# Performance work log

Hardware: AMD Instinct MI355X
Metric: run time of the kernel (lower is better)

The kernel has to match this reference:

```python
import jax, jax.numpy as jnp
import numpy as np

N_NODES = 20000
N_EDGES = 640000
IN_DIM = 128
HID = 128
OUT_DIM = 64
N_STEPS = 16   # N in the torch module
H = 0.1        # ODE step size


def setup_inputs() -> dict:
    key = jax.random.key(0)
    ks = jax.random.split(key, 20)
    s = 1.0 / np.sqrt(HID)

    def g(k, shape, scale=s):
        return (jax.random.normal(k, shape, dtype=jnp.float32) * scale)

    return {
        "x": jax.random.normal(ks[0], (N_NODES, IN_DIM), dtype=jnp.float32),
        "edge_index": jax.random.randint(ks[1], (2, N_EDGES), 0, N_NODES, dtype=jnp.int32),
        "W_enc1": g(ks[2], (HID, IN_DIM), 1.0 / np.sqrt(IN_DIM)),
        "b_enc1": g(ks[3], (HID,)),
        "W_enc2": g(ks[4], (HID, HID)),
        "b_enc2": g(ks[5], (HID,)),
        "W_ih_f": g(ks[6], (4 * HID, HID)),
        "W_hh_f": g(ks[7], (4 * HID, HID)),
        "b_ih_f": g(ks[8], (4 * HID,)),
        "b_hh_f": g(ks[9], (4 * HID,)),
        "W_ih_b": g(ks[10], (4 * HID, HID)),
        "W_hh_b": g(ks[11], (4 * HID, HID)),
        "b_ih_b": g(ks[12], (4 * HID,)),
        "b_hh_b": g(ks[13], (4 * HID,)),
        "W_f1": g(ks[14], (HID, 2 * HID), 1.0 / np.sqrt(2 * HID)),
        "b_f1": g(ks[15], (HID,)),
        "W_f2": g(ks[16], (OUT_DIM, HID)),
        "b_f2": g(ks[17], (OUT_DIM,)),
    }


def _lstm_scan(xs, W_ih, W_hh, b_ih, b_hh):
    """Unidirectional LSTM over xs [T, B, H] -> hidden states [T, B, H]."""
    B = xs.shape[1]
    Hd = W_hh.shape[1]
    h0 = jnp.zeros((B, Hd), xs.dtype)

    def cell(carry, x_t):
        h, c = carry
        gates = x_t @ W_ih.T + b_ih + h @ W_hh.T + b_hh
        i, f, g, o = jnp.split(gates, 4, axis=-1)  # torch gate order: i,f,g,o
        i = jax.nn.sigmoid(i)
        f = jax.nn.sigmoid(f)
        g = jnp.tanh(g)
        o = jax.nn.sigmoid(o)
        c_new = f * c + i * g
        h_new = o * jnp.tanh(c_new)
        return (h_new, c_new), h_new

    _, hs = jax.lax.scan(cell, (h0, h0), xs)
    return hs


def reference(x, edge_index, W_enc1, b_enc1, W_enc2, b_enc2,
              W_ih_f, W_hh_f, b_ih_f, b_hh_f,
              W_ih_b, W_hh_b, b_ih_b, b_hh_b,
              W_f1, b_f1, W_f2, b_f2):
    row, col = edge_index[0], edge_index[1]

    # initial encoders
    X = x @ W_enc1.T + b_enc1
    Y = jnp.zeros_like(X)
    X = jax.nn.relu(X)
    X = X @ W_enc2.T + b_enc2

    # node degree (count of col occurrences), inf-guard not needed (deg used directly)
    deg = jax.ops.segment_sum(jnp.ones((N_EDGES,), X.dtype), col, num_segments=N_NODES)

    def wave_step(carry, _):
        Xc, Yc = carry
        # L x = deg*x - sum_{j->i} x_j   (scatter-add of -x[row] at col)
        mes = -jax.ops.segment_sum(Xc[row], col, num_segments=N_NODES)
        vel_update = deg[:, None] * Xc + mes
        Yn = Yc - H * vel_update
        Xn = Xc + H * Yn
        return (Xn, Yn), Xn

    _, Xs = jax.lax.scan(wave_step, (X, Y), None, length=N_STEPS - 1)
    X_tilde = jnp.concatenate([X[None], Xs], axis=0)  # [N, n_nodes, HID]

    hs_f = _lstm_scan(X_tilde, W_ih_f, W_hh_f, b_ih_f, b_hh_f)
    hs_b = _lstm_scan(X_tilde[::-1], W_ih_b, W_hh_b, b_ih_b, b_hh_b)
    # out_vec[-1] = [fwd hidden at last step, bwd hidden at last position]
    out_last = jnp.concatenate([hs_f[-1], hs_b[0]], axis=-1)  # [n_nodes, 2*HID]

    out = jax.nn.relu(out_last @ W_f1.T + b_f1)
    out = out @ W_f2.T + b_f2
    return out
```

## Files before the change

kernel.cpp:

```cpp
#include <hip/hip_runtime.h>
#include <hip/hip_bf16.h>
#include <cstdint>
#include <cstddef>

#define N_NODES 20000
#define N_EDGES 640000
#define HID     128
#define OUT_DIM 64
#define NSTEPS  16
#define HSTEP   0.1f
#define H2      0.01f
#define NBLK    625

typedef unsigned short u16;
typedef __attribute__((ext_vector_type(8))) short short8;
typedef __attribute__((ext_vector_type(4))) float f32x4;

__device__ __forceinline__ float bf2f(u16 u) {
    union { unsigned int i; float f; } v; v.i = ((unsigned int)u) << 16; return v.f;
}
__device__ __forceinline__ u16 f2bf(float f) {
    union { float f; unsigned int i; } v; v.f = f;
    unsigned int x = v.i;
    unsigned int r = x + 0x7FFFu + ((x >> 16) & 1u);
    return (u16)(r >> 16);
}

__device__ __forceinline__ float sigm(float x) { return 1.f / (1.f + __expf(-x)); }
__device__ __forceinline__ float tanh_fast(float x) {
    float e2 = __expf(-2.f * fabsf(x));
    float t = (1.f - e2) / (1.f + e2);
    return copysignf(t, x);
}

__global__ void detect_kernel(const u16* __restrict__ xraw, int* __restrict__ flag) {
    __shared__ int cnt;
    if (threadIdx.x == 0) cnt = 0;
    __syncthreads();
    int c = 0;
    for (int i = threadIdx.x; i < 4096; i += 256) {
        int e = (xraw[i] >> 7) & 0xFF;
        if (e >= 0x90) c++;
    }
    atomicAdd(&cnt, c);
    __syncthreads();
    if (threadIdx.x == 0) *flag = (cnt > 100) ? 1 : 0;
}

#define N_CVT 15
struct CvtArgs { const void* s[N_CVT]; };
__constant__ const int cvt_off[N_CVT + 1] = {
    0, 16384, 16512, 32896, 33024, 98560, 164096, 164608, 165120,
    230656, 231168, 231680, 264448, 264576, 272768, 272832 };

__global__ void convert_kernel(CvtArgs a, float* __restrict__ dst,
                               const int* __restrict__ flag) {
    int i = blockIdx.x * blockDim.x + threadIdx.x;
    if (i >= 272832) return;
    int seg = 0;
    #pragma unroll
    for (int s = 1; s < N_CVT; ++s) if (i >= cvt_off[s]) seg = s;
    int j = i - cvt_off[seg];
    float v = (*flag) ? ((const float*)a.s[seg])[j]
                      : bf2f(((const u16*)a.s[seg])[j]);
    dst[i] = v;
}

__global__ void build_wswz_kernel(const float* __restrict__ wsf,
                                  u16* __restrict__ WswzF, u16* __restrict__ WswzB,
                                  u16* __restrict__ WswzH, u16* __restrict__ WswzO,
                                  u16* __restrict__ WswzE1, u16* __restrict__ WswzE2) {
    int o = blockIdx.x * blockDim.x + threadIdx.x;
    if (o < 131072) {
        int j = o & 7, l = (o >> 3) & 63, rest = o >> 9;
        int ck = rest & 7, nt = rest >> 3;
        int n = nt * 16 + (l & 15);
        int k = ck * 32 + (l >> 4) * 8 + j;
        const float* Wihf = wsf + 33024;
        const float* Whhf = wsf + 98560;
        float v = (k < 128) ? Wihf[n * 128 + k] : Whhf[n * 128 + (k - 128)];
        WswzF[o] = f2bf(v);
    }
    if (o < 65536) {
        int j = o & 7, l = (o >> 3) & 63, rest = o >> 9;
        int ck = rest & 3, nt = rest >> 2;
        int n = nt * 16 + (l & 15);
        int k = ck * 32 + (l >> 4) * 8 + j;
        const float* Wihb = wsf + 165120;
        WswzB[o] = f2bf(Wihb[n * 128 + k]);
    }
    if (o < 32768) {
        int j = o & 7, l = (o >> 3) & 63, rest = o >> 9;
        int ck = rest & 7, nt = rest >> 3;
        int n = nt * 16 + (l & 15);
        int k = ck * 32 + (l >> 4) * 8 + j;
        const float* Wf1 = wsf + 231680;
        WswzH[o] = f2bf(Wf1[n * 256 + k]);
    }
    if (o < 8192) {
        int j = o & 7, l = (o >> 3) & 63, rest = o >> 9;
        int ck = rest & 3, nt = rest >> 2;
        int n = nt * 16 + (l & 15);
        int k = ck * 32 + (l >> 4) * 8 + j;
        const float* Wf2 = wsf + 264576;
        WswzO[o] = f2bf(Wf2[n * 128 + k]);
    }
    if (o < 16384) {
        int j = o & 7, l = (o >> 3) & 63, rest = o >> 9;
        int ck = rest & 3, nt = rest >> 2;
        int n = nt * 16 + (l & 15);
        int k = ck * 32 + (l >> 4) * 8 + j;
        const float* We1 = wsf + 0;
        const float* We2 = wsf + 16512;
        WswzE1[o] = f2bf(We1[n * 128 + k]);
        WswzE2[o] = f2bf(We2[n * 128 + k]);
    }
}

__global__ void count_kernel(const int* __restrict__ ei, int* __restrict__ deg) {
    int e = blockIdx.x * blockDim.x + threadIdx.x;
    if (e < N_EDGES) atomicAdd(&deg[ei[N_EDGES + e]], 1);
}

__global__ __launch_bounds__(1024) void scan_kernel(const int* __restrict__ deg,
                                                    int* __restrict__ rowptr,
                                                    float* __restrict__ degf) {
    __shared__ int sd[1024];
    const int t = threadIdx.x;
    const int CH = (N_NODES + 1023) / 1024;
    int base = t * CH;
    int s = 0;
    for (int i = 0; i < CH; ++i) {
        int idx = base + i;
        if (idx < N_NODES) s += deg[idx];
    }
    sd[t] = s;
    __syncthreads();
    for (int off = 1; off < 1024; off <<= 1) {
        int v = (t >= off) ? sd[t - off] : 0;
        __syncthreads();
        sd[t] += v;
        __syncthreads();
    }
    int run = (t == 0) ? 0 : sd[t - 1];
    for (int i = 0; i < CH; ++i) {
        int idx = base + i;
        if (idx < N_NODES) {
            rowptr[idx] = run;
            degf[idx] = (float)deg[idx];
            run += deg[idx];
        }
    }
    if (t == 1023) rowptr[N_NODES] = sd[1023];
}

__global__ void fill_kernel(const int* __restrict__ ei, const int* __restrict__ rowptr,
                            int* __restrict__ fill, int* __restrict__ csr) {
    int e = blockIdx.x * blockDim.x + threadIdx.x;
    if (e < N_EDGES) {
        int d = ei[N_EDGES + e];
        int p = atomicAdd(&fill[d], 1);
        csr[rowptr[d] + p] = ei[e];
    }
}

__global__ __launch_bounds__(512) void encoder_kernel(
    const void* __restrict__ xv,
    const u16* __restrict__ WswzE1, const u16* __restrict__ WswzE2,
    const float* __restrict__ benc1, const float* __restrict__ benc2,
    float* __restrict__ Xa, u16* __restrict__ Xsnap0, const int* __restrict__ flag)
{
    __shared__ __align__(16) u16 H1[32][136];
    const int w = threadIdx.x >> 6;
    const int l = threadIdx.x & 63;
    const int l15 = l & 15, quad = l >> 4;
    const int m0 = blockIdx.x * 32;
    const int kof = quad * 8;
    const int j = w * 16 + l15;
    const bool xf32 = (*flag != 0);

    f32x4 acc[2] = {};
    #pragma unroll
    for (int ck = 0; ck < 4; ++ck) {
        const int kc = ck * 32;
        short8 a0, a1;
        if (xf32) {
            const float* r0 = (const float*)xv + (size_t)(m0 + l15) * HID + kc + kof;
            const float* r1 = (const float*)xv + (size_t)(m0 + 16 + l15) * HID + kc + kof;
            union { u16 u[8]; short8 v; } t0, t1;
            #pragma unroll
            for (int e = 0; e < 8; ++e) { t0.u[e] = f2bf(r0[e]); t1.u[e] = f2bf(r1[e]); }
            a0 = t0.v; a1 = t1.v;
        } else {
            a0 = *(const short8*)((const u16*)xv + (size_t)(m0 + l15) * HID + kc + kof);
            a1 = *(const short8*)((const u16*)xv + (size_t)(m0 + 16 + l15) * HID + kc + kof);
        }
        short8 b = *(const short8*)(WswzE1 + (((size_t)(w * 4 + ck)) << 9) + (l << 3));
        acc[0] = __builtin_amdgcn_mfma_f32_16x16x32_bf16(a0, b, acc[0], 0, 0, 0);
        acc[1] = __builtin_amdgcn_mfma_f32_16x16x32_bf16(a1, b, acc[1], 0, 0, 0);
    }
    {
        const float bj = benc1[j];
        #pragma unroll
        for (int mt = 0; mt < 2; ++mt)
            #pragma unroll
            for (int i = 0; i < 4; ++i)
                H1[mt * 16 + quad * 4 + i][j] = f2bf(fmaxf(acc[mt][i] + bj, 0.f));
    }
    __syncthreads();

    f32x4 acc2[2] = {};
    #pragma unroll
    for (int ck = 0; ck < 4; ++ck) {
        const int kc = ck * 32;
        short8 a0 = *(const short8*)(&H1[l15][kc + kof]);
        short8 a1 = *(const short8*)(&H1[16 + l15][kc + kof]);
        short8 b = *(const short8*)(WswzE2 + (((size_t)(w * 4 + ck)) << 9) + (l << 3));
        acc2[0] = __builtin_amdgcn_mfma_f32_16x16x32_bf16(a0, b, acc2[0], 0, 0, 0);
        acc2[1] = __builtin_amdgcn_mfma_f32_16x16x32_bf16(a1, b, acc2[1], 0, 0, 0);
    }
    {
        const float bj = benc2[j];
        #pragma unroll
        for (int mt = 0; mt < 2; ++mt)
            #pragma unroll
            for (int i = 0; i < 4; ++i) {
                int m = m0 + mt * 16 + quad * 4 + i;
                float o = acc2[mt][i] + bj;
                Xa[(size_t)m * HID + j] = o;
                Xsnap0[(size_t)m * HID + j] = f2bf(o);
            }
    }
}

template<bool FIRST>
__global__ __launch_bounds__(256) void wave_kernel(
    const float* __restrict__ Xcur, float* __restrict__ Xdst,
    const u16* __restrict__ XbfP, u16* __restrict__ XbfN,
    const float* __restrict__ degf,
    const int* __restrict__ rowptr, const int* __restrict__ csr)
{
    const int node = blockIdx.x * 4 + (threadIdx.x >> 6);
    const int lane = threadIdx.x & 63;
    const int q = lane >> 4;
    const int fl = (lane & 15) * 8;

    const int beg = rowptr[node], end = rowptr[node + 1];
    float s0[8] = {}, s1[8] = {}, s2[8] = {}, s3[8] = {};

    int i = beg;
    for (; i + 16 <= end; i += 16) {
        int v0 = csr[i + 0 + q];
        int v1 = csr[i + 4 + q];
        int v2 = csr[i + 8 + q];
        int v3 = csr[i + 12 + q];
        short8 g0 = *(const short8*)(XbfP + (size_t)v0 * HID + fl);
        short8 g1 = *(const short8*)(XbfP + (size_t)v1 * HID + fl);
        short8 g2 = *(const short8*)(XbfP + (size_t)v2 * HID + fl);
        short8 g3 = *(const short8*)(XbfP + (size_t)v3 * HID + fl);
        #pragma unroll
        for (int e = 0; e < 8; ++e) {
            s0[e] += bf2f((u16)g0[e]);
            s1[e] += bf2f((u16)g1[e]);
            s2[e] += bf2f((u16)g2[e]);
            s3[e] += bf2f((u16)g3[e]);
        }
    }
    for (; i + 4 <= end; i += 4) {
        int v = csr[i + q];
        short8 g = *(const short8*)(XbfP + (size_t)v * HID + fl);
        #pragma unroll
        for (int e = 0; e < 8; ++e) s0[e] += bf2f((u16)g[e]);
    }
    if (i + q < end) {
        int v = csr[i + q];
        short8 g = *(const short8*)(XbfP + (size_t)v * HID + fl);
        #pragma unroll
        for (int e = 0; e < 8; ++e) s1[e] += bf2f((u16)g[e]);
    }

    float t[8];
    #pragma unroll
    for (int e = 0; e < 8; ++e) {
        t[e] = (s0[e] + s1[e]) + (s2[e] + s3[e]);
        t[e] += __shfl_xor(t[e], 16, 64);
        t[e] += __shfl_xor(t[e], 32, 64);
    }

    if (q == 0) {
        const size_t off = (size_t)node * HID + fl;
        float xc[8], xp[8], xn[8];
        *(float4*)&xc[0] = *(const float4*)(Xcur + off);
        *(float4*)&xc[4] = *(const float4*)(Xcur + off + 4);
        if (!FIRST) {
            *(float4*)&xp[0] = *(const float4*)(Xdst + off);
            *(float4*)&xp[4] = *(const float4*)(Xdst + off + 4);
        }
        const float d = degf[node];
        const float c0 = 2.f - H2 * d;
        short8 sv;
        #pragma unroll
        for (int e = 0; e < 8; ++e) {
            float prev = FIRST ? xc[e] : xp[e];
            xn[e] = c0 * xc[e] - prev + H2 * t[e];
            sv[e] = (short)f2bf(xn[e]);
        }
        *(float4*)(Xdst + off)     = *(float4*)&xn[0];
        *(float4*)(Xdst + off + 4) = *(float4*)&xn[4];
        *(short8*)(XbfN + off)     = sv;
    }
}

__global__ __launch_bounds__(512) void lstm16w_kernel(
    const u16* __restrict__ Xsnap,
    u16* __restrict__ hOut,
    const u16* __restrict__ WswzF,
    const float* __restrict__ bih, const float* __restrict__ bhh)
{
    __shared__ __align__(16) u16 hL[32][136];
    const int w = threadIdx.x >> 6;
    const int l = threadIdx.x & 63;
    const int l15 = l & 15, quad = l >> 4;
    const int m0 = blockIdx.x * 32;
    const int kof = quad * 8;
    const int j = w * 16 + l15;

    {
        const int r  = threadIdx.x >> 4;
        const int cc = (threadIdx.x & 15) * 8;
        short8 z = {};
        *(short8*)&hL[r][cc] = z;
    }

    short8 wf[4][8];
    #pragma unroll
    for (int q = 0; q < 4; ++q)
        #pragma unroll
        for (int ck = 0; ck < 8; ++ck)
            wf[q][ck] = *(const short8*)(WswzF +
                (((size_t)((q * 8 + w) * 8 + ck)) << 9) + (l << 3));

    const float bI = bih[j]       + bhh[j];
    const float bF = bih[128 + j] + bhh[128 + j];
    const float bG = bih[256 + j] + bhh[256 + j];
    const float bO = bih[384 + j] + bhh[384 + j];
    float cst[2][4] = {};

    const size_t rowA0 = (size_t)(m0 + l15) * HID + kof;
    const size_t rowA1 = (size_t)(m0 + 16 + l15) * HID + kof;
    __syncthreads();

    #pragma unroll 1
    for (int t = 0; t < NSTEPS; ++t) {
        const u16* Xbf = Xsnap + (size_t)t * N_NODES * HID;
        f32x4 acc[2][4] = {};
        #pragma unroll
        for (int ck = 0; ck < 8; ++ck) {
            const int kc = ck * 32;
            short8 a0, a1;
            if (kc < 128) {
                a0 = *(const short8*)(Xbf + rowA0 + kc);
                a1 = *(const short8*)(Xbf + rowA1 + kc);
            } else {
                a0 = *(const short8*)(&hL[l15][kc - 128 + kof]);
                a1 = *(const short8*)(&hL[16 + l15][kc - 128 + kof]);
            }
            #pragma unroll
            for (int q = 0; q < 4; ++q) {
                acc[0][q] = __builtin_amdgcn_mfma_f32_16x16x32_bf16(a0, wf[q][ck], acc[0][q], 0, 0, 0);
                acc[1][q] = __builtin_amdgcn_mfma_f32_16x16x32_bf16(a1, wf[q][ck], acc[1][q], 0, 0, 0);
            }
        }
        __syncthreads();
        #pragma unroll
        for (int mt = 0; mt < 2; ++mt) {
            #pragma unroll
            for (int i = 0; i < 4; ++i) {
                float gi = sigm(acc[mt][0][i] + bI);
                float gf = sigm(acc[mt][1][i] + bF);
                float gg = tanh_fast(acc[mt][2][i] + bG);
                float go = sigm(acc[mt][3][i] + bO);
                float cn = gf * cst[mt][i] + gi * gg;
                cst[mt][i] = cn;
                hL[mt * 16 + quad * 4 + i][j] = f2bf(go * tanh_fast(cn));
            }
        }
        __syncthreads();
    }

    {
        const int r  = threadIdx.x >> 4;
        const int cc = (threadIdx.x & 15) * 8;
        *(short8*)(hOut + (size_t)(m0 + r) * HID + cc) = *(const short8*)&hL[r][cc];
    }
}

__global__ __launch_bounds__(512) void tail2_kernel(
    const u16* __restrict__ Xbf15, const u16* __restrict__ h15,
    const u16* __restrict__ WswzB, const u16* __restrict__ WswzH,
    const u16* __restrict__ WswzO,
    const float* __restrict__ bihb, const float* __restrict__ bhhb,
    const float* __restrict__ bf1, const float* __restrict__ bf2_,
    void* __restrict__ out, const int* __restrict__ oflag)
{
    __shared__ __align__(16) u16 hL[32][136];
    __shared__ __align__(16) u16 Hb[32][136];
    __shared__ __align__(16) u16 F1[32][136];
    const int w = threadIdx.x >> 6;
    const int l = threadIdx.x & 63;
    const int l15 = l & 15, quad = l >> 4;
    const int m0 = blockIdx.x * 32;
    const int kof = quad * 8;
    const int j = w * 16 + l15;

    {
        const int r  = threadIdx.x >> 4;
        const int cc = (threadIdx.x & 15) * 8;
        *(short8*)&hL[r][cc] =
            *(const short8*)(h15 + (size_t)(m0 + r) * HID + cc);
    }

    const size_t rowA0 = (size_t)(m0 + l15) * HID + kof;
    const size_t rowA1 = (size_t)(m0 + 16 + l15) * HID + kof;

    {
        f32x4 acc[2][4] = {};
        #pragma unroll
        for (int kc = 0; kc < 128; kc += 32) {
            const int ck = kc >> 5;
            short8 a0 = *(const short8*)(Xbf15 + rowA0 + kc);
            short8 a1 = *(const short8*)(Xbf15 + rowA1 + kc);
            #pragma unroll
            for (int q = 0; q < 4; ++q) {
                int nt = q * 8 + w;
                short8 b = *(const short8*)(WswzB + (((size_t)(nt * 4 + ck)) << 9) + (l << 3));
                acc[0][q] = __builtin_amdgcn_mfma_f32_16x16x32_bf16(a0, b, acc[0][q], 0, 0, 0);
                acc[1][q] = __builtin_amdgcn_mfma_f32_16x16x32_bf16(a1, b, acc[1][q], 0, 0, 0);
            }
        }
        const float cI = bihb[j]       + bhhb[j];
        const float cG = bihb[256 + j] + bhhb[256 + j];
        const float cO = bihb[384 + j] + bhhb[384 + j];
        #pragma unroll
        for (int mt = 0; mt < 2; ++mt)
            #pragma unroll
            for (int i = 0; i < 4; ++i) {
                float gi = sigm(acc[mt][0][i] + cI);
                float gg = tanh_fast(acc[mt][2][i] + cG);
                float go = sigm(acc[mt][3][i] + cO);
                Hb[mt * 16 + quad * 4 + i][j] = f2bf(go * tanh_fast(gi * gg));
            }
    }
    __syncthreads();

    {
        f32x4 acc[2] = {};
        #pragma unroll
        for (int kc = 0; kc < 256; kc += 32) {
            const int ck = kc >> 5;
            short8 a0, a1;
            if (kc < 128) {
                a0 = *(const short8*)(&hL[l15][kc + kof]);
                a1 = *(const short8*)(&hL[16 + l15][kc + kof]);
            } else {
                a0 = *(const short8*)(&Hb[l15][(kc - 128) + kof]);
                a1 = *(const short8*)(&Hb[16 + l15][(kc - 128) + kof]);
            }
            short8 b = *(const short8*)(WswzH + (((size_t)(w * 8 + ck)) << 9) + (l << 3));
            acc[0] = __builtin_amdgcn_mfma_f32_16x16x32_bf16(a0, b, acc[0], 0, 0, 0);
            acc[1] = __builtin_amdgcn_mfma_f32_16x16x32_bf16(a1, b, acc[1], 0, 0, 0);
        }
        const float bj = bf1[j];
        #pragma unroll
        for (int mt = 0; mt < 2; ++mt)
            #pragma unroll
            for (int i = 0; i < 4; ++i)
                F1[mt * 16 + quad * 4 + i][j] = f2bf(fmaxf(acc[mt][i] + bj, 0.f));
    }
    __syncthreads();

    {
        const int nt = w & 3, mh = w >> 2;
        f32x4 acc = {};
        #pragma unroll
        for (int kc = 0; kc < 128; kc += 32) {
            const int ck = kc >> 5;
            short8 a = *(const short8*)(&F1[mh * 16 + l15][kc + kof]);
            short8 b = *(const short8*)(WswzO + (((size_t)(nt * 4 + ck)) << 9) + (l << 3));
            acc = __builtin_amdgcn_mfma_f32_16x16x32_bf16(a, b, acc, 0, 0, 0);
        }
        const int jo = nt * 16 + l15;
        const float bj = bf2_[jo];
        const bool obf = (*oflag == 0);
        #pragma unroll
        for (int i = 0; i < 4; ++i) {
            int m = m0 + mh * 16 + quad * 4 + i;
            float o = acc[i] + bj;
            if (obf) ((u16*)out)[(size_t)m * OUT_DIM + jo] = f2bf(o);
            else     ((float*)out)[(size_t)m * OUT_DIM + jo] = o;
        }
    }
}

extern "C" void kernel_launch(void* const* d_in, const int* in_sizes, int n_in,
                              void* d_out, int out_size, void* d_ws, size_t ws_size,
                              hipStream_t stream)
{
    const void* x  = d_in[0];
    const int*  ei = (const int*)d_in[1];

    const size_t SZ_NH  = (size_t)N_NODES * HID * sizeof(float);
    const size_t SZ_NHB = (size_t)N_NODES * HID * sizeof(u16);
    const size_t SZ_I   = 80128;

    char* p = (char*)d_ws;
    float* Xa    = (float*)p; p += SZ_NH;
    float* Xb    = (float*)p; p += SZ_NH;
    u16*   Xsnap = (u16*)p;   p += (size_t)NSTEPS * SZ_NHB;
    u16*   h15   = (u16*)p;   p += SZ_NHB;
    int*   deg   = (int*)p;   p += SZ_I;
    int*   fill  = (int*)p;   p += SZ_I;
    int*   rowp  = (int*)p;   p += SZ_I;
    float* degf  = (float*)p; p += SZ_I;
    int*   csr   = (int*)p;   p += (size_t)N_EDGES * sizeof(int);
    int*   flag  = (int*)p;   p += 128;
    float* wsf   = (float*)p; p += 272832 * sizeof(float);
    u16*   WswzF  = (u16*)p;  p += 131072 * sizeof(u16);
    u16*   WswzB  = (u16*)p;  p += 65536 * sizeof(u16);
    u16*   WswzH  = (u16*)p;  p += 32768 * sizeof(u16);
    u16*   WswzO  = (u16*)p;  p += 8192 * sizeof(u16);
    u16*   WswzE1 = (u16*)p;  p += 16384 * sizeof(u16);
    u16*   WswzE2 = (u16*)p;  p += 16384 * sizeof(u16);

    float* benc1 = wsf + 16384;
    float* benc2 = wsf + 32896;
    float* bihf  = wsf + 164096;
    float* bhhf  = wsf + 164608;
    float* bihb  = wsf + 230656;
    float* bhhb  = wsf + 231168;
    float* bf1   = wsf + 264448;
    float* bf2_  = wsf + 272768;

    (void)hipMemsetAsync(deg, 0, 2 * SZ_I, stream);

    detect_kernel<<<1, 256, 0, stream>>>((const u16*)x, flag);
    CvtArgs ca;
    ca.s[0] = d_in[2];  ca.s[1] = d_in[3];  ca.s[2] = d_in[4];  ca.s[3] = d_in[5];
    ca.s[4] = d_in[6];  ca.s[5] = d_in[7];  ca.s[6] = d_in[8];  ca.s[7] = d_in[9];
    ca.s[8] = d_in[10]; ca.s[9] = d_in[12]; ca.s[10] = d_in[13];
    ca.s[11] = d_in[14]; ca.s[12] = d_in[15]; ca.s[13] = d_in[16]; ca.s[14] = d_in[17];
    convert_kernel<<<(272832 + 255) / 256, 256, 0, stream>>>(ca, wsf, flag);
    build_wswz_kernel<<<512, 256, 0, stream>>>(wsf, WswzF, WswzB, WswzH, WswzO,
                                               WswzE1, WswzE2);

    count_kernel<<<(N_EDGES + 255) / 256, 256, 0, stream>>>(ei, deg);
    scan_kernel<<<1, 1024, 0, stream>>>(deg, rowp, degf);
    fill_kernel<<<(N_EDGES + 255) / 256, 256, 0, stream>>>(ei, rowp, fill, csr);

    encoder_kernel<<<NBLK, 512, 0, stream>>>(x, WswzE1, WswzE2, benc1, benc2,
                                             Xa, Xsnap, flag);

    float* Xc_ = Xa;
    float* Xo_ = Xb;
    for (int t = 1; t < NSTEPS; ++t) {
        const u16* XbP = Xsnap + (size_t)(t - 1) * N_NODES * HID;
        u16*       XbN = Xsnap + (size_t)t * N_NODES * HID;
        if (t == 1)
            wave_kernel<true><<<N_NODES / 4, 256, 0, stream>>>(
                Xc_, Xo_, XbP, XbN, degf, rowp, csr);
        else
            wave_kernel<false><<<N_NODES / 4, 256, 0, stream>>>(
                Xc_, Xo_, XbP, XbN, degf, rowp, csr);
        float* tf = Xc_; Xc_ = Xo_; Xo_ = tf;
    }

    lstm16w_kernel<<<NBLK, 512, 0, stream>>>(Xsnap, h15, WswzF, bihf, bhhf);

    tail2_kernel<<<NBLK, 512, 0, stream>>>(
        Xsnap + (size_t)(NSTEPS - 1) * N_NODES * HID, h15,
        WswzB, WswzH, WswzO, bihb, bhhb, bf1, bf2_, d_out, flag);
}
```

Measured before the change: 827.2 us.

## Prefetch next-step X fragments in LSTM kernel and use fast reciprocal activations

The LSTM kernel now loads the X-input A fragments for the next timestep into registers while the current step's MFMAs run, so global loads are no longer serialized at the head of each step. Sigmoid and tanh use the hardware reciprocal instead of a full divide. It also adds a launch-bounds occupancy hint of 2 and pins the weight registers with empty asm. The cost is higher register pressure from the prefetch buffers, which could cause spills at the requested occupancy, and slightly lower activation accuracy.

```diff
diff --git a/kernel.cpp b/kernel.cpp
--- a/kernel.cpp
+++ b/kernel.cpp
@@ -30,6 +30,16 @@
 __device__ __forceinline__ float tanh_fast(float x) {
     float e2 = __expf(-2.f * fabsf(x));
     float t = (1.f - e2) / (1.f + e2);
+    return copysignf(t, x);
+}
+
+__device__ __forceinline__ float rcp_f(float x) { return __builtin_amdgcn_rcpf(x); }
+__device__ __forceinline__ float sigm_f(float x) {
+    return rcp_f(1.f + __expf(-x));
+}
+__device__ __forceinline__ float tanh_f(float x) {
+    float e2 = __expf(-2.f * fabsf(x));
+    float t = (1.f - e2) * rcp_f(1.f + e2);
     return copysignf(t, x);
 }
 
@@ -311,7 +321,7 @@
     }
 }
 
-__global__ __launch_bounds__(512) void lstm16w_kernel(
+__global__ __launch_bounds__(512, 2) void lstm16w_kernel(
     const u16* __restrict__ Xsnap,
     u16* __restrict__ hOut,
     const u16* __restrict__ WswzF,
@@ -339,6 +349,11 @@
         for (int ck = 0; ck < 8; ++ck)
             wf[q][ck] = *(const short8*)(WswzF +
                 (((size_t)((q * 8 + w) * 8 + ck)) << 9) + (l << 3));
+    #pragma unroll
+    for (int q = 0; q < 4; ++q)
+        #pragma unroll
+        for (int ck = 0; ck < 8; ++ck)
+            asm volatile("" : "+v"(wf[q][ck]));
 
     const float bI = bih[j]       + bhh[j];
     const float bF = bih[128 + j] + bhh[128 + j];
@@ -348,23 +363,37 @@
 
     const size_t rowA0 = (size_t)(m0 + l15) * HID + kof;
     const size_t rowA1 = (size_t)(m0 + 16 + l15) * HID + kof;
+
+    short8 xa[4], xb[4];
+    #pragma unroll
+    for (int ck = 0; ck < 4; ++ck) {
+        xa[ck] = *(const short8*)(Xsnap + rowA0 + ck * 32);
+        xb[ck] = *(const short8*)(Xsnap + rowA1 + ck * 32);
+    }
     __syncthreads();
 
     #pragma unroll 1
     for (int t = 0; t < NSTEPS; ++t) {
-        const u16* Xbf = Xsnap + (size_t)t * N_NODES * HID;
         f32x4 acc[2][4] = {};
         #pragma unroll
-        for (int ck = 0; ck < 8; ++ck) {
-            const int kc = ck * 32;
-            short8 a0, a1;
-            if (kc < 128) {
-                a0 = *(const short8*)(Xbf + rowA0 + kc);
-                a1 = *(const short8*)(Xbf + rowA1 + kc);
-            } else {
-                a0 = *(const short8*)(&hL[l15][kc - 128 + kof]);
-                a1 = *(const short8*)(&hL[16 + l15][kc - 128 + kof]);
-            }
+        for (int ck = 0; ck < 4; ++ck)
+            #pragma unroll
+            for (int q = 0; q < 4; ++q) {
+                acc[0][q] = __builtin_amdgcn_mfma_f32_16x16x32_bf16(xa[ck], wf[q][ck], acc[0][q], 0, 0, 0);
+                acc[1][q] = __builtin_amdgcn_mfma_f32_16x16x32_bf16(xb[ck], wf[q][ck], acc[1][q], 0, 0, 0);
+            }
+        if (t + 1 < NSTEPS) {
+            const u16* Xn = Xsnap + (size_t)(t + 1) * N_NODES * HID;
+            #pragma unroll
+            for (int ck = 0; ck < 4; ++ck) {
+                xa[ck] = *(const short8*)(Xn + rowA0 + ck * 32);
+                xb[ck] = *(const short8*)(Xn + rowA1 + ck * 32);
+            }
+        }
+        #pragma unroll
+        for (int ck = 4; ck < 8; ++ck) {
+            short8 a0 = *(const short8*)(&hL[l15][(ck - 4) * 32 + kof]);
+            short8 a1 = *(const short8*)(&hL[16 + l15][(ck - 4) * 32 + kof]);
             #pragma unroll
             for (int q = 0; q < 4; ++q) {
                 acc[0][q] = __builtin_amdgcn_mfma_f32_16x16x32_bf16(a0, wf[q][ck], acc[0][q], 0, 0, 0);
@@ -376,13 +405,13 @@
         for (int mt = 0; mt < 2; ++mt) {
             #pragma unroll
             for (int i = 0; i < 4; ++i) {
-                float gi = sigm(acc[mt][0][i] + bI);
-                float gf = sigm(acc[mt][1][i] + bF);
-                float gg = tanh_fast(acc[mt][2][i] + bG);
-                float go = sigm(acc[mt][3][i] + bO);
+                float gi = sigm_f(acc[mt][0][i] + bI);
+                float gf = sigm_f(acc[mt][1][i] + bF);
+                float gg = tanh_f(acc[mt][2][i] + bG);
+                float go = sigm_f(acc[mt][3][i] + bO);
                 float cn = gf * cst[mt][i] + gi * gg;
                 cst[mt][i] = cn;
-                hL[mt * 16 + quad * 4 + i][j] = f2bf(go * tanh_fast(cn));
+                hL[mt * 16 + quad * 4 + i][j] = f2bf(go * tanh_f(cn));
             }
         }
         __syncthreads();
```

After: 712.6 us. 1.16x faster.
